# Optimization experiments

Hardware: AMD Instinct MI355X
Metric: run time of the kernel (lower is better)

The kernel has to match this reference:

```python
import jax, jax.numpy as jnp
import numpy as np

SPLINE_ORDER = 3
GRID_SIZE = 1
# efficient-kan style grid over [-1,1], extended by spline_order on each side; h = 2/grid_size = 2
GRID = jnp.arange(-SPLINE_ORDER, GRID_SIZE + SPLINE_ORDER + 1, dtype=jnp.float32) * 2.0 - 1.0
NB = GRID_SIZE + SPLINE_ORDER  # 4 basis functions per input feature
EPS = 1e-5


def b_splines(x, grid):
    # x: [..., in] -> [..., in, NB] via Cox-de Boor recursion
    xe = x[..., None]
    b = ((xe >= grid[:-1]) & (xe < grid[1:])).astype(x.dtype)
    for p in range(1, SPLINE_ORDER + 1):
        b = ((xe - grid[:-(p + 1)]) / (grid[p:-1] - grid[:-(p + 1)]) * b[..., :-1]
             + (grid[p + 1:] - xe) / (grid[p + 1:] - grid[1:-p]) * b[..., 1:])
    return b


def kan_linear(x, base_w, spline_w):
    # base branch: silu(x) @ W_base^T ; spline branch: B(x) contracted with W_spline [out,in,NB]
    base = jnp.einsum('...i,oi->...o', jax.nn.silu(x), base_w)
    sp = jnp.einsum('...ik,oik->...o', b_splines(x, GRID), spline_w)
    return base + sp


def kan_conv2x2(x, base_w, spline_w):
    # x: [B,C,H,W] -> [B,C_out,H-1,W-1]
    p = jax.lax.conv_general_dilated_patches(x, (2, 2), (1, 1), 'VALID')  # [B, C*4, H', W']
    p = jnp.moveaxis(p, 1, -1)  # [B,H',W',C*4]
    y = kan_linear(p, base_w, spline_w)  # [B,H',W',C_out]
    return jnp.moveaxis(y, -1, 1)


def bn2d(x, g, b):
    m = x.mean((0, 2, 3), keepdims=True)
    v = x.var((0, 2, 3), keepdims=True)
    return (x - m) * jax.lax.rsqrt(v + EPS) * g[None, :, None, None] + b[None, :, None, None]


def bn1d(x, g, b):
    m = x.mean(0, keepdims=True)
    v = x.var(0, keepdims=True)
    return (x - m) * jax.lax.rsqrt(v + EPS) * g[None, :] + b[None, :]


def maxpool2(x):
    B, C, H, W = x.shape
    Hc, Wc = (H // 2) * 2, (W // 2) * 2
    return x[:, :, :Hc, :Wc].reshape(B, C, H // 2, 2, W // 2, 2).max((3, 5))


def setup_inputs() -> dict:
    key = jax.random.key(0)
    ks = jax.random.split(key, 16)
    f32 = jnp.float32
    d = {
        'x': jax.random.normal(ks[0], (1024, 3, 32, 32), f32),
        'base_w1': jax.random.normal(ks[1], (32, 12), f32) * 0.2,
        'spline_w1': jax.random.normal(ks[2], (32, 12, NB), f32) * 0.1,
        'bn1_g': jnp.ones((32,), f32), 'bn1_b': jnp.zeros((32,), f32),
        'base_w2': jax.random.normal(ks[3], (64, 128), f32) * 0.08,
        'spline_w2': jax.random.normal(ks[4], (64, 128, NB), f32) * 0.04,
        'bn2_g': jnp.ones((64,), f32), 'bn2_b': jnp.zeros((64,), f32),
        'fc1_w': jax.random.normal(ks[5], (64, 3136), f32) * 0.02,
        'fc1_b': jnp.zeros((64,), f32),
        'bn3_g': jnp.ones((64,), f32), 'bn3_b': jnp.zeros((64,), f32),
        'fc2_w': jax.random.normal(ks[6], (10, 64), f32) * 0.1,
        'fc2_b': jnp.zeros((10,), f32),
    }
    return d


def reference(x, base_w1, spline_w1, bn1_g, bn1_b, base_w2, spline_w2, bn2_g, bn2_b,
              fc1_w, fc1_b, bn3_g, bn3_b, fc2_w, fc2_b):
    h = kan_conv2x2(x, base_w1, spline_w1)            # [B,32,31,31]
    h = jax.nn.relu(bn2d(h, bn1_g, bn1_b))
    h = maxpool2(h)                                   # [B,32,15,15]
    h = kan_conv2x2(h, base_w2, spline_w2)            # [B,64,14,14]
    h = jax.nn.relu(bn2d(h, bn2_g, bn2_b))
    h = maxpool2(h)                                   # [B,64,7,7]
    h = h.reshape(h.shape[0], -1)                     # [B,3136]
    h = h @ fc1_w.T + fc1_b
    h = jax.nn.relu(bn1d(h, bn3_g, bn3_b))
    # Dropout is identity at inference
    return h @ fc2_w.T + fc2_b                        # [B,10]
```

## Files before the change

kernel.cpp:

```cpp
#include <hip/hip_runtime.h>
#include <math.h>

#define BN_EPS 1e-5f

typedef __attribute__((ext_vector_type(8))) _Float16 f16x8;
typedef __attribute__((ext_vector_type(4))) _Float16 f16x4;
typedef __attribute__((ext_vector_type(2))) __fp16 fp16v2;
typedef __attribute__((ext_vector_type(4))) float f32x4;


__device__ __forceinline__ float siluf(float v) {
    return v * __builtin_amdgcn_rcpf(1.0f + __expf(-v));
}

__device__ __forceinline__ void expand5(float v, float f[5]) {
    f[0] = siluf(v);
    float u = (v + 7.0f) * 0.5f;
#pragma unroll
    for (int i = 0; i < 4; ++i) {
        float a = fabsf(u - (float)(i + 2));
        float p = fmaxf(2.0f - a, 0.0f);
        float q = fmaxf(1.0f - a, 0.0f);
        f[i + 1] = p * p * p - 4.0f * (q * q * q);
    }
}

__device__ __forceinline__ int pkh(float a, float b) {
    union { fp16v2 h2; int i; } u;
    u.h2 = __builtin_amdgcn_cvt_pkrtz(a, b);
    return u.i;
}


__global__ __launch_bounds__(256) void prep_kernel(
        const float* __restrict__ fw1, unsigned int* __restrict__ wTh2,
        const float* __restrict__ bw2, const float* __restrict__ sw2,
        _Float16* __restrict__ Wf,
        const float* __restrict__ bw1, const float* __restrict__ sw1,
        _Float16* __restrict__ Wf1) {
    int blk = blockIdx.x;
    if (blk < 392) {
        int t = blk * 256 + threadIdx.x;
        int o = t & 63;
        int j2 = t >> 6;
        int jc = (j2 * 2) & 63;
        int q2 = (j2 * 2) >> 6;
        wTh2[t] = (unsigned int)pkh(fw1[(size_t)o * 3136 + jc * 49 + q2],
                                    fw1[(size_t)o * 3136 + (jc + 1) * 49 + q2]);
    } else if (blk < 552) {
        int t = (blk - 392) * 256 + threadIdx.x;
        if (t >= 64 * 640) return;
        int n = t / 640;
        int k = t - n * 640;
        int s = k / 160;
        int r = k - s * 160;
        int f = r >> 5;
        int c = r & 31;
        float val = (f == 0) ? bw2[n * 128 + c * 4 + s]
                             : sw2[n * 512 + c * 16 + s * 4 + (f - 1)] * (1.0f / 6.0f);
        Wf[t] = (_Float16)val;
    } else {
        int t = (blk - 552) * 256 + threadIdx.x;
        if (t >= 32 * 64) return;
        int n = t >> 6;
        int k = t & 63;
        int s = k >> 4, j = k & 15;
        float val = 0.f;
        if (j < 15) {
            int f = j / 3, c = j - f * 3;
            int i = c * 4 + s;
            val = (f == 0) ? bw1[n * 12 + i]
                           : sw1[(n * 12 + i) * 4 + f - 1] * (1.0f / 6.0f);
        }
        Wf1[t] = (_Float16)val;
    }
}


__global__ __launch_bounds__(256, 4) void conv1_kernel(
        const float* __restrict__ x, const _Float16* __restrict__ Wf1,
        _Float16* __restrict__ pooled, float* __restrict__ part) {
    __shared__ _Float16 Eu[1025 * 16];
    __shared__ float Rs[4][64];
    char* EuB = (char*)Eu;

    int t = threadIdx.x;
    int lane = t & 63, wv = t >> 6;
    int quad = lane >> 4, l15 = lane & 15;
    int b = blockIdx.x;

    const _Float16* wb0 = Wf1 + (size_t)l15 * 64 + quad * 8;
    f16x8 bf00 = *(const f16x8*)(wb0);
    f16x8 bf01 = *(const f16x8*)(wb0 + 32);
    f16x8 bf10 = *(const f16x8*)(wb0 + 16 * 64);
    f16x8 bf11 = *(const f16x8*)(wb0 + 16 * 64 + 32);

    float xv[12];
    const float* xb = x + (size_t)b * 3072;
#pragma unroll
    for (int k = 0; k < 12; ++k) xv[k] = xb[t + k * 256];
#pragma unroll
    for (int k = 0; k < 12; ++k) {
        int idx = t + k * 256;
        int c = idx >> 10;
        int pos = idx & 1023;
        float f[5];
        expand5(xv[k], f);
        int rb = pos * 32;
        int key = (pos & 12) << 2;
        *(_Float16*)(EuB + ((rb + c * 2) ^ key))        = (_Float16)f[0];
        *(_Float16*)(EuB + ((rb + (3 + c) * 2) ^ key))  = (_Float16)f[1];
        *(_Float16*)(EuB + ((rb + (6 + c) * 2) ^ key))  = (_Float16)f[2];
        *(_Float16*)(EuB + ((rb + (9 + c) * 2) ^ key))  = (_Float16)f[3];
        *(_Float16*)(EuB + ((rb + (12 + c) * 2) ^ key)) = (_Float16)f[4];
    }
    if (t < 8) *(int*)(EuB + 32768 + t * 4) = 0;
    __syncthreads();

    int dxq = quad >> 1, hb = (quad & 1) * 16;
    int wxv = 8 * wv + (l15 & 7);
    int colb = wxv + dxq;
    int pbase = (colb * 32 + hb) ^ ((colb & 12) << 2);
    bool vx = wxv < 31;
    int pzero = 32768 + hb;
    int wy0 = l15 >> 3;

    float ss0 = 0.f, sq0 = 0.f, ss1 = 0.f, sq1 = 0.f;

    int p0 = vx ? wy0 * 1024 + pbase : pzero;
    f16x8 a0 = *(const f16x8*)(EuB + p0);
    f16x8 a1 = *(const f16x8*)(EuB + p0 + (vx ? 1024 : 0));

#pragma unroll 1
    for (int i = 0; i < 16; ++i) {
        f32x4 acc0 = (f32x4){0.f, 0.f, 0.f, 0.f};
        f32x4 acc1 = (f32x4){0.f, 0.f, 0.f, 0.f};
        acc0 = __builtin_amdgcn_mfma_f32_16x16x32_f16(a0, bf00, acc0, 0, 0, 0);
        acc1 = __builtin_amdgcn_mfma_f32_16x16x32_f16(a0, bf10, acc1, 0, 0, 0);
        acc0 = __builtin_amdgcn_mfma_f32_16x16x32_f16(a1, bf01, acc0, 0, 0, 0);
        acc1 = __builtin_amdgcn_mfma_f32_16x16x32_f16(a1, bf11, acc1, 0, 0, 0);
        if (i < 15) {
            int wyn = 2 * (i + 1) + wy0;
            bool vn = vx && (wyn < 31);
            int pn = vn ? wyn * 1024 + pbase : pzero;
            a0 = *(const f16x8*)(EuB + pn);
            a1 = *(const f16x8*)(EuB + pn + (vn ? 1024 : 0));
        }
        float h00 = fmaxf(acc0[0], acc0[1]);
        float h01 = fmaxf(acc0[2], acc0[3]);
        float h10 = fmaxf(acc1[0], acc1[1]);
        float h11 = fmaxf(acc1[2], acc1[3]);
        float g00 = fmaxf(h00, __shfl_down(h00, 32, 64));
        float g01 = fmaxf(h01, __shfl_down(h01, 32, 64));
        float g10 = fmaxf(h10, __shfl_down(h10, 32, 64));
        float g11 = fmaxf(h11, __shfl_down(h11, 32, 64));
        if (lane < 32 && i < 15) {
            int pn0 = 4 * wv + (quad & 1) * 2;
            size_t base = ((size_t)b * 225 + i * 15) * 32;
            if (pn0 < 15) {
                pooled[base + pn0 * 32 + l15]      = (_Float16)g00;
                pooled[base + pn0 * 32 + 16 + l15] = (_Float16)g10;
            }
            if (pn0 < 14) {
                pooled[base + (pn0 + 1) * 32 + l15]      = (_Float16)g01;
                pooled[base + (pn0 + 1) * 32 + 16 + l15] = (_Float16)g11;
            }
        }
        ss0 += acc0[0] + acc0[1] + acc0[2] + acc0[3];
        sq0 += acc0[0] * acc0[0] + acc0[1] * acc0[1]
             + acc0[2] * acc0[2] + acc0[3] * acc0[3];
        ss1 += acc1[0] + acc1[1] + acc1[2] + acc1[3];
        sq1 += acc1[0] * acc1[0] + acc1[1] * acc1[1]
             + acc1[2] * acc1[2] + acc1[3] * acc1[3];
    }

    ss0 += __shfl_down(ss0, 32, 64); ss0 += __shfl_down(ss0, 16, 64);
    sq0 += __shfl_down(sq0, 32, 64); sq0 += __shfl_down(sq0, 16, 64);
    ss1 += __shfl_down(ss1, 32, 64); ss1 += __shfl_down(ss1, 16, 64);
    sq1 += __shfl_down(sq1, 32, 64); sq1 += __shfl_down(sq1, 16, 64);
    if (lane < 16) {
        Rs[wv][2 * l15]          = ss0;
        Rs[wv][2 * l15 + 1]      = sq0;
        Rs[wv][32 + 2 * l15]     = ss1;
        Rs[wv][32 + 2 * l15 + 1] = sq1;
    }
    __syncthreads();
    if (t < 64)
        part[(size_t)b * 64 + t] = Rs[0][t] + Rs[1][t] + Rs[2][t] + Rs[3][t];
}


#define EU_PS 200

__device__ __forceinline__ void c2_loadb(const _Float16* __restrict__ Wb,
                                         int g, f16x8 bf[5]) {
#pragma unroll
    for (int ks = 0; ks < 5; ++ks)
        bf[ks] = *(const f16x8*)(Wb + g * 160 + ks * 32);
}

__device__ __forceinline__ void c2_mfma(const _Float16* Eu,
                                        const int abase[4][4], int g,
                                        int quad, const f16x8 bf[5],
                                        f32x4 acc[4]) {
#pragma unroll
    for (int ks = 0; ks < 5; ++ks) {
        int jo = ks * 40 + quad * 8;
#pragma unroll
        for (int mt = 0; mt < 4; ++mt) {
            f16x8 a = *(const f16x8*)&Eu[abase[mt][g] + jo];
            acc[mt] = __builtin_amdgcn_mfma_f32_16x16x32_f16(a, bf[ks], acc[mt], 0, 0, 0);
        }
    }
}

__global__ __launch_bounds__(256, 6) void conv2_kernel(
        const _Float16* __restrict__ pooled, const float* __restrict__ stats1,
        const float* __restrict__ g1v, const float* __restrict__ b1v,
        const _Float16* __restrict__ Wf, _Float16* __restrict__ Pt,
        float* __restrict__ part) {
    __shared__ _Float16 Eu[65 * EU_PS];

    int t = threadIdx.x;
    int lane = t & 63, wv = t >> 6;
    int quad = lane >> 4, l15 = lane & 15;

    int blk = blockIdx.x;
    int b = blk >> 2;
    int py0 = ((blk >> 1) & 1) * 7;
    int px0 = (blk & 1) * 7;

    const _Float16* Wb = Wf + (size_t)(wv * 16 + l15) * 640 + quad * 8;
    f16x8 bfA[5], bfB[5];
    c2_loadb(Wb, 0, bfA);

    {
        int c2 = t & 15, c0 = c2 * 2;
        int xx = (t >> 4) & 7;
        int yh = t >> 7;
        const float invN1 = 1.0f / (1024.0f * 961.0f);
        float m0 = stats1[2 * c0] * invN1;
        float v0 = stats1[2 * c0 + 1] * invN1 - m0 * m0;
        float sc0 = rsqrtf(v0 + BN_EPS) * g1v[c0];
        float sh0 = b1v[c0] - m0 * sc0;
        float m1 = stats1[2 * c0 + 2] * invN1;
        float v1 = stats1[2 * c0 + 3] * invN1 - m1 * m1;
        float sc1 = rsqrtf(v1 + BN_EPS) * g1v[c0 + 1];
        float sh1 = b1v[c0 + 1] - m1 * sc1;
        const _Float16* pbase0 =
            pooled + ((size_t)b * 225 + py0 * 15 + px0) * 32 + c0;
#pragma unroll
        for (int yi = 0; yi < 4; ++yi) {
            int yr = yh * 4 + yi;
            fp16v2 v2 = *(const fp16v2*)(pbase0 + yr * 480 + xx * 32);
            float va = fmaxf((float)v2.x * sc0 + sh0, 0.f);
            float vb = fmaxf((float)v2.y * sc1 + sh1, 0.f);
            float fa[5], fb5[5];
            expand5(va, fa);
            expand5(vb, fb5);
            int* eb = (int*)&Eu[(yr * 8 + xx) * EU_PS] + c2;
            eb[0]  = pkh(fa[0], fb5[0]);
            eb[20] = pkh(fa[1], fb5[1]);
            eb[40] = pkh(fa[2], fb5[2]);
            eb[60] = pkh(fa[3], fb5[3]);
            eb[80] = pkh(fa[4], fb5[4]);
        }
    }
    if (t < 100) ((int*)&Eu[64 * EU_PS])[t] = 0;

    int abase[4][4];
#pragma unroll
    for (int mt = 0; mt < 4; ++mt) {
        int m = mt * 16 + l15;
        if (m < 49) {
            int pr = m / 7, pc = m - pr * 7;
#pragma unroll
            for (int s = 0; s < 4; ++s)
                abase[mt][s] = ((pr + (s >> 1)) * 8 + pc + (s & 1)) * EU_PS;
        } else {
#pragma unroll
            for (int s = 0; s < 4; ++s) abase[mt][s] = 64 * EU_PS;
        }
    }
    __syncthreads();

    f32x4 acc[4];
#pragma unroll
    for (int mt = 0; mt < 4; ++mt) acc[mt] = (f32x4){0.f, 0.f, 0.f, 0.f};

    c2_loadb(Wb, 1, bfB);
    c2_mfma(Eu, abase, 0, quad, bfA, acc);
    c2_loadb(Wb, 2, bfA);
    c2_mfma(Eu, abase, 1, quad, bfB, acc);
    c2_loadb(Wb, 3, bfB);
    c2_mfma(Eu, abase, 2, quad, bfA, acc);
    c2_mfma(Eu, abase, 3, quad, bfB, acc);

    int o = wv * 16 + l15;
#pragma unroll
    for (int mt = 0; mt < 4; ++mt) {
#pragma unroll
        for (int reg = 0; reg < 4; ++reg) {
            int m = mt * 16 + quad * 4 + reg;
            if (m < 49) {
                int pr = m / 7, pc = m - pr * 7;
                int patch = (b * 14 + py0 + pr) * 14 + px0 + pc;
                Pt[(size_t)patch * 64 + o] = (_Float16)acc[mt][reg];
            }
        }
    }
    float s = 0.f, s2 = 0.f;
#pragma unroll
    for (int mt = 0; mt < 4; ++mt)
#pragma unroll
        for (int reg = 0; reg < 4; ++reg) {
            float a = acc[mt][reg];
            s += a;
            s2 += a * a;
        }
    s  += __shfl_down(s, 16, 64);  s  += __shfl_down(s, 32, 64);
    s2 += __shfl_down(s2, 16, 64); s2 += __shfl_down(s2, 32, 64);
    if (lane < 16) {
        part[(size_t)blk * 128 + 2 * o]     = s;
        part[(size_t)blk * 128 + 2 * o + 1] = s2;
    }
}


__global__ __launch_bounds__(256) void redstats_kernel(
        const float* __restrict__ part, float* __restrict__ stats,
        int nblk, int stride) {
    int p = blockIdx.x;
    float s = 0.f;
    for (int j = threadIdx.x; j < nblk; j += 256)
        s += part[(size_t)j * stride + p];
#pragma unroll
    for (int off = 32; off > 0; off >>= 1) s += __shfl_down(s, off, 64);
    __shared__ float ls[4];
    if ((threadIdx.x & 63) == 0) ls[threadIdx.x >> 6] = s;
    __syncthreads();
    if (threadIdx.x == 0) stats[p] = ls[0] + ls[1] + ls[2] + ls[3];
}


__global__ __launch_bounds__(256) void bnpool2_kernel(
        const _Float16* __restrict__ Pt, const float* __restrict__ stats,
        const float* __restrict__ g, const float* __restrict__ bb,
        _Float16* __restrict__ out) {
    int t = blockIdx.x * 256 + threadIdx.x;
    if (t >= 1024 * 49 * 16) return;
    int c4 = (t & 15) * 4;
    int q2 = (t >> 4) % 49;
    int b  = t / (49 * 16);
    float sc[4], sh[4];
#pragma unroll
    for (int j = 0; j < 4; ++j) {
        int c = c4 + j;
        float mean = stats[2 * c] * (1.0f / 200704.0f);
        float var  = stats[2 * c + 1] * (1.0f / 200704.0f) - mean * mean;
        sc[j] = rsqrtf(var + BN_EPS) * g[c];
        sh[j] = bb[c] - mean * sc[j];
    }
    int py2 = q2 / 7, px2 = q2 - py2 * 7;
    int q = (py2 * 2) * 14 + px2 * 2;
    const _Float16* p = Pt + ((size_t)b * 196 + q) * 64 + c4;
    f16x4 r0 = *(const f16x4*)(p);
    f16x4 r1 = *(const f16x4*)(p + 64);
    f16x4 r2 = *(const f16x4*)(p + 14 * 64);
    f16x4 r3 = *(const f16x4*)(p + 15 * 64);
    f16x4 res;
#pragma unroll
    for (int j = 0; j < 4; ++j) {
        float v0 = fmaxf((float)r0[j] * sc[j] + sh[j], 0.f);
        float v1 = fmaxf((float)r1[j] * sc[j] + sh[j], 0.f);
        float v2 = fmaxf((float)r2[j] * sc[j] + sh[j], 0.f);
        float v3 = fmaxf((float)r3[j] * sc[j] + sh[j], 0.f);
        res[j] = (_Float16)fmaxf(fmaxf(v0, v1), fmaxf(v2, v3));
    }
    *(f16x4*)(out + (size_t)b * 3136 + q2 * 64 + c4) = res;
}


__global__ __launch_bounds__(256) void fc1_kernel(
        const _Float16* __restrict__ xin, const unsigned int* __restrict__ wTh2,
        const float* __restrict__ bias, float* __restrict__ z) {
    __shared__ unsigned int xsu[2 * 1568];
    __shared__ float red[2][4][64];
    int b0 = blockIdx.x * 2;
    const unsigned int* xg = (const unsigned int*)xin + (size_t)b0 * 1568;
    for (int j = threadIdx.x; j < 2 * 1568; j += 256) xsu[j] = xg[j];
    __syncthreads();
    int o = threadIdx.x & 63, q = threadIdx.x >> 6;
    float s0 = 0.f, s1 = 0.f;
    const unsigned int* wp = wTh2 + (size_t)q * 392 * 64 + o;
    int jb = q * 392;
    for (int i = 0; i < 392; ++i) {
        union { unsigned int u; fp16v2 h; } uw, u0, u1;
        uw.u = wp[i * 64];
        u0.u = xsu[jb + i];
        u1.u = xsu[1568 + jb + i];
        s0 = __builtin_amdgcn_fdot2(u0.h, uw.h, s0, false);
        s1 = __builtin_amdgcn_fdot2(u1.h, uw.h, s1, false);
    }
    red[0][q][o] = s0; red[1][q][o] = s1;
    __syncthreads();
    if (threadIdx.x < 128) {
        int bb = threadIdx.x >> 6;
        int oo = threadIdx.x & 63;
        float tot = red[bb][0][oo] + red[bb][1][oo] + red[bb][2][oo]
                  + red[bb][3][oo] + bias[oo];
        z[((size_t)(b0 + bb)) * 64 + oo] = tot;
    }
}


__global__ __launch_bounds__(256) void colstats_kernel(
        const float* __restrict__ z, const float* __restrict__ g,
        const float* __restrict__ bb, float* __restrict__ scsh) {
    int c = blockIdx.x;
    float s = 0.f, s2 = 0.f;
    for (int b = threadIdx.x; b < 1024; b += 256) {
        float v = z[(size_t)b * 64 + c];
        s += v; s2 += v * v;
    }
#pragma unroll
    for (int off = 32; off > 0; off >>= 1) {
        s  += __shfl_down(s, off, 64);
        s2 += __shfl_down(s2, off, 64);
    }
    __shared__ float ls[8];
    int w = threadIdx.x >> 6;
    if ((threadIdx.x & 63) == 0) { ls[w * 2] = s; ls[w * 2 + 1] = s2; }
    __syncthreads();
    if (threadIdx.x == 0) {
        float st = ls[0] + ls[2] + ls[4] + ls[6];
        float st2 = ls[1] + ls[3] + ls[5] + ls[7];
        float mean = st * (1.0f / 1024.0f);
        float var  = st2 * (1.0f / 1024.0f) - mean * mean;
        float sc = rsqrtf(var + BN_EPS) * g[c];
        scsh[2 * c]     = sc;
        scsh[2 * c + 1] = bb[c] - mean * sc;
    }
}


__global__ __launch_bounds__(256) void final_kernel(
        const float* __restrict__ z, const float* __restrict__ scsh,
        const float* __restrict__ w2, const float* __restrict__ b2,
        float* __restrict__ out) {
    int t = blockIdx.x * 256 + threadIdx.x;
    if (t >= 10240) return;
    int o = t % 10, b = t / 10;
    float acc = b2[o];
#pragma unroll 8
    for (int c = 0; c < 64; ++c) {
        float a = fmaxf(z[(size_t)b * 64 + c] * scsh[2 * c] + scsh[2 * c + 1], 0.f);
        acc += a * w2[o * 64 + c];
    }
    out[t] = acc;
}


extern "C" void kernel_launch(void* const* d_in, const int* in_sizes, int n_in,
                              void* d_out, int out_size, void* d_ws, size_t ws_size,
                              hipStream_t stream) {
    const float* x   = (const float*)d_in[0];
    const float* bw1 = (const float*)d_in[1];
    const float* sw1 = (const float*)d_in[2];
    const float* g1  = (const float*)d_in[3];
    const float* b1  = (const float*)d_in[4];
    const float* bw2 = (const float*)d_in[5];
    const float* sw2 = (const float*)d_in[6];
    const float* g2  = (const float*)d_in[7];
    const float* b2v = (const float*)d_in[8];
    const float* fw1 = (const float*)d_in[9];
    const float* fb1 = (const float*)d_in[10];
    const float* g3  = (const float*)d_in[11];
    const float* b3  = (const float*)d_in[12];
    const float* fw2 = (const float*)d_in[13];
    const float* fb2 = (const float*)d_in[14];
    float* out = (float*)d_out;

    char* ws = (char*)d_ws;
    float* part1     = (float*)(ws);
    _Float16* Pt     = (_Float16*)(ws);
    float* part2     = (float*)(ws + 51380224);
    _Float16* Wf     = (_Float16*)(ws + 100000000);
    _Float16* Wf1    = (_Float16*)(ws + 100131072);
    _Float16* pooled = (_Float16*)(ws + 125960192);
    float* z         = (float*)(ws + 155451392);
    unsigned int* wTh2 = (unsigned int*)(ws + 155713536);
    float* stats1    = (float*)(ws + 156516352);
    float* stats2    = (float*)(ws + 156516608);
    float* stats3    = (float*)(ws + 156517120);

    prep_kernel<<<560, 256, 0, stream>>>(fw1, wTh2, bw2, sw2, Wf, bw1, sw1, Wf1);

    conv1_kernel<<<1024, 256, 0, stream>>>(x, Wf1, pooled, part1);
    redstats_kernel<<<64, 256, 0, stream>>>(part1, stats1, 1024, 64);

    conv2_kernel<<<4096, 256, 0, stream>>>(pooled, stats1, g1, b1,
                                           Wf, Pt, part2);
    redstats_kernel<<<128, 256, 0, stream>>>(part2, stats2, 4096, 128);

    _Float16* pooled2 = pooled;
    bnpool2_kernel<<<(1024 * 49 * 16 + 255) / 256, 256, 0, stream>>>(
        Pt, stats2, g2, b2v, pooled2);

    fc1_kernel<<<512, 256, 0, stream>>>(pooled2, wTh2, fb1, z);
    colstats_kernel<<<64, 256, 0, stream>>>(z, g3, b3, stats3);
    final_kernel<<<(10240 + 255) / 256, 256, 0, stream>>>(z, stats3, fw2, fb2, out);
}
```

Baseline: 190.2 us.

## Use 32x32 MFMA tiles in conv2 and parallelize stats reduction with atomics

Conv2 now uses 32x32x16 MFMA with a 2x2 wave split over rows and output channels, and a software-pipelined loop that prefetches the next A and B fragments. The aim is to cut LDS reads and redundant weight loads per MFMA and raise matrix-core efficiency. Partial stats are combined in shared memory before being written. The redstats kernel now does a coalesced, grid-wide strided sum followed by atomicAdd into stats that prep_kernel zeroes, replacing strided per-column loops that used few blocks. This makes float summation order nondeterministic.

```diff
diff --git a/kernel.cpp b/kernel.cpp
--- a/kernel.cpp
+++ b/kernel.cpp
@@ -7,6 +7,7 @@
 typedef __attribute__((ext_vector_type(4))) _Float16 f16x4;
 typedef __attribute__((ext_vector_type(2))) __fp16 fp16v2;
 typedef __attribute__((ext_vector_type(4))) float f32x4;
+typedef __attribute__((ext_vector_type(16))) float f32x16;
 
 
 __device__ __forceinline__ float siluf(float v) {
@@ -37,7 +38,8 @@
         const float* __restrict__ bw2, const float* __restrict__ sw2,
         _Float16* __restrict__ Wf,
         const float* __restrict__ bw1, const float* __restrict__ sw1,
-        _Float16* __restrict__ Wf1) {
+        _Float16* __restrict__ Wf1,
+        float* __restrict__ stats1, float* __restrict__ stats2) {
     int blk = blockIdx.x;
     if (blk < 392) {
         int t = blk * 256 + threadIdx.x;
@@ -60,7 +62,12 @@
                              : sw2[n * 512 + c * 16 + s * 4 + (f - 1)] * (1.0f / 6.0f);
         Wf[t] = (_Float16)val;
     } else {
-        int t = (blk - 552) * 256 + threadIdx.x;
+        int tid = threadIdx.x;
+        if (blk == 559) {
+            if (tid < 64) stats1[tid] = 0.f;
+            else if (tid < 192) stats2[tid - 64] = 0.f;
+        }
+        int t = (blk - 552) * 256 + tid;
         if (t >= 32 * 64) return;
         int n = t >> 6;
         int k = t & 63;
@@ -192,47 +199,26 @@
 
 #define EU_PS 200
 
-__device__ __forceinline__ void c2_loadb(const _Float16* __restrict__ Wb,
-                                         int g, f16x8 bf[5]) {
-#pragma unroll
-    for (int ks = 0; ks < 5; ++ks)
-        bf[ks] = *(const f16x8*)(Wb + g * 160 + ks * 32);
-}
-
-__device__ __forceinline__ void c2_mfma(const _Float16* Eu,
-                                        const int abase[4][4], int g,
-                                        int quad, const f16x8 bf[5],
-                                        f32x4 acc[4]) {
-#pragma unroll
-    for (int ks = 0; ks < 5; ++ks) {
-        int jo = ks * 40 + quad * 8;
-#pragma unroll
-        for (int mt = 0; mt < 4; ++mt) {
-            f16x8 a = *(const f16x8*)&Eu[abase[mt][g] + jo];
-            acc[mt] = __builtin_amdgcn_mfma_f32_16x16x32_f16(a, bf[ks], acc[mt], 0, 0, 0);
-        }
-    }
-}
-
 __global__ __launch_bounds__(256, 6) void conv2_kernel(
         const _Float16* __restrict__ pooled, const float* __restrict__ stats1,
         const float* __restrict__ g1v, const float* __restrict__ b1v,
         const _Float16* __restrict__ Wf, _Float16* __restrict__ Pt,
         float* __restrict__ part) {
     __shared__ _Float16 Eu[65 * EU_PS];
+    __shared__ float Rs[4][64];
 
     int t = threadIdx.x;
     int lane = t & 63, wv = t >> 6;
-    int quad = lane >> 4, l15 = lane & 15;
+    int l31 = lane & 31, kl = (lane >> 5) * 8;
+    int mw = wv >> 1, nw = wv & 1;
 
     int blk = blockIdx.x;
     int b = blk >> 2;
     int py0 = ((blk >> 1) & 1) * 7;
     int px0 = (blk & 1) * 7;
 
-    const _Float16* Wb = Wf + (size_t)(wv * 16 + l15) * 640 + quad * 8;
-    f16x8 bfA[5], bfB[5];
-    c2_loadb(Wb, 0, bfA);
+    const _Float16* Wb = Wf + (size_t)(nw * 32 + l31) * 640 + kl;
+    f16x8 bF = *(const f16x8*)(Wb);
 
     {
         int c2 = t & 15, c0 = c2 * 2;
@@ -268,78 +254,86 @@
     }
     if (t < 100) ((int*)&Eu[64 * EU_PS])[t] = 0;
 
-    int abase[4][4];
-#pragma unroll
-    for (int mt = 0; mt < 4; ++mt) {
-        int m = mt * 16 + l15;
+    int arow = mw * 32 + l31;
+    int abase[4];
+    if (arow < 49) {
+        int pr = arow / 7, pc = arow - pr * 7;
+#pragma unroll
+        for (int s = 0; s < 4; ++s)
+            abase[s] = ((pr + (s >> 1)) * 8 + pc + (s & 1)) * EU_PS + kl;
+    } else {
+#pragma unroll
+        for (int s = 0; s < 4; ++s) abase[s] = 64 * EU_PS + kl;
+    }
+    __syncthreads();
+
+    f32x16 acc;
+#pragma unroll
+    for (int i = 0; i < 16; ++i) acc[i] = 0.f;
+
+    f16x8 aF = *(const f16x8*)&Eu[abase[0]];
+    f16x8 aN, bN;
+#pragma unroll
+    for (int kk = 0; kk < 40; ++kk) {
+        if (kk < 39) {
+            const int k2 = kk + 1;
+            const int s2 = k2 / 10, r2 = k2 - s2 * 10, f2 = r2 >> 1, c2 = r2 & 1;
+            aN = *(const f16x8*)&Eu[abase[s2] + f2 * 40 + c2 * 16];
+            bN = *(const f16x8*)(Wb + s2 * 160 + f2 * 32 + c2 * 16);
+        }
+        acc = __builtin_amdgcn_mfma_f32_32x32x16_f16(aF, bF, acc, 0, 0, 0);
+        aF = aN;
+        bF = bN;
+    }
+
+    int col = nw * 32 + l31;
+#pragma unroll
+    for (int r = 0; r < 16; ++r) {
+        int rloc = (r & 3) + 8 * (r >> 2) + 4 * (lane >> 5);
+        int m = mw * 32 + rloc;
         if (m < 49) {
             int pr = m / 7, pc = m - pr * 7;
-#pragma unroll
-            for (int s = 0; s < 4; ++s)
-                abase[mt][s] = ((pr + (s >> 1)) * 8 + pc + (s & 1)) * EU_PS;
-        } else {
-#pragma unroll
-            for (int s = 0; s < 4; ++s) abase[mt][s] = 64 * EU_PS;
-        }
-    }
-    __syncthreads();
-
-    f32x4 acc[4];
-#pragma unroll
-    for (int mt = 0; mt < 4; ++mt) acc[mt] = (f32x4){0.f, 0.f, 0.f, 0.f};
-
-    c2_loadb(Wb, 1, bfB);
-    c2_mfma(Eu, abase, 0, quad, bfA, acc);
-    c2_loadb(Wb, 2, bfA);
-    c2_mfma(Eu, abase, 1, quad, bfB, acc);
-    c2_loadb(Wb, 3, bfB);
-    c2_mfma(Eu, abase, 2, quad, bfA, acc);
-    c2_mfma(Eu, abase, 3, quad, bfB, acc);
-
-    int o = wv * 16 + l15;
-#pragma unroll
-    for (int mt = 0; mt < 4; ++mt) {
-#pragma unroll
-        for (int reg = 0; reg < 4; ++reg) {
-            int m = mt * 16 + quad * 4 + reg;
-            if (m < 49) {
-                int pr = m / 7, pc = m - pr * 7;
-                int patch = (b * 14 + py0 + pr) * 14 + px0 + pc;
-                Pt[(size_t)patch * 64 + o] = (_Float16)acc[mt][reg];
-            }
+            int patch = (b * 14 + py0 + pr) * 14 + px0 + pc;
+            Pt[(size_t)patch * 64 + col] = (_Float16)acc[r];
         }
     }
     float s = 0.f, s2 = 0.f;
 #pragma unroll
-    for (int mt = 0; mt < 4; ++mt)
-#pragma unroll
-        for (int reg = 0; reg < 4; ++reg) {
-            float a = acc[mt][reg];
-            s += a;
-            s2 += a * a;
-        }
-    s  += __shfl_down(s, 16, 64);  s  += __shfl_down(s, 32, 64);
-    s2 += __shfl_down(s2, 16, 64); s2 += __shfl_down(s2, 32, 64);
-    if (lane < 16) {
-        part[(size_t)blk * 128 + 2 * o]     = s;
-        part[(size_t)blk * 128 + 2 * o + 1] = s2;
+    for (int r = 0; r < 16; ++r) {
+        float a = acc[r];
+        s += a;
+        s2 += a * a;
+    }
+    s  += __shfl_down(s, 32, 64);
+    s2 += __shfl_down(s2, 32, 64);
+    if (lane < 32) {
+        Rs[wv][2 * l31]     = s;
+        Rs[wv][2 * l31 + 1] = s2;
+    }
+    __syncthreads();
+    if (t < 128) {
+        int o = t >> 1;
+        int nwv = o >> 5;
+        int lidx = (o & 31) * 2 + (t & 1);
+        part[(size_t)blk * 128 + t] = Rs[nwv][lidx] + Rs[nwv + 2][lidx];
     }
 }
 
 
 __global__ __launch_bounds__(256) void redstats_kernel(
         const float* __restrict__ part, float* __restrict__ stats,
-        int nblk, int stride) {
-    int p = blockIdx.x;
-    float s = 0.f;
-    for (int j = threadIdx.x; j < nblk; j += 256)
-        s += part[(size_t)j * stride + p];
-#pragma unroll
-    for (int off = 32; off > 0; off >>= 1) s += __shfl_down(s, off, 64);
-    __shared__ float ls[4];
-    if ((threadIdx.x & 63) == 0) ls[threadIdx.x >> 6] = s;
-    __syncthreads();
-    if (threadIdx.x == 0) stats[p] = ls[0] + ls[1] + ls[2] + ls[3];
+        int total, int width) {
+    float acc = 0.f;
+    for (int i = blockIdx.x * 256 + threadIdx.x; i < total; i += gridDim.x * 256)
+        acc += part[i];
+    __shared__ float ls[256];
+    ls[threadIdx.x] = acc;
+    __syncthreads();
+    if (threadIdx.x < width) {
+        float v = ls[threadIdx.x];
+        for (int j = threadIdx.x + width; j < 256; j += width) v += ls[j];
+        atomicAdd(&stats[threadIdx.x], v);
+    }
 }
 
 
@@ -494,14 +488,15 @@
     float* stats2    = (float*)(ws + 156516608);
     float* stats3    = (float*)(ws + 156517120);
 
-    prep_kernel<<<560, 256, 0, stream>>>(fw1, wTh2, bw2, sw2, Wf, bw1, sw1, Wf1);
+    prep_kernel<<<560, 256, 0, stream>>>(fw1, wTh2, bw2, sw2, Wf, bw1, sw1, Wf1,
+                                         stats1, stats2);
 
     conv1_kernel<<<1024, 256, 0, stream>>>(x, Wf1, pooled, part1);
-    redstats_kernel<<<64, 256, 0, stream>>>(part1, stats1, 1024, 64);
+    redstats_kernel<<<256, 256, 0, stream>>>(part1, stats1, 1024 * 64, 64);
 
     conv2_kernel<<<4096, 256, 0, stream>>>(pooled, stats1, g1, b1,
                                            Wf, Pt, part2);
-    redstats_kernel<<<128, 256, 0, stream>>>(part2, stats2, 4096, 128);
+    redstats_kernel<<<512, 256, 0, stream>>>(part2, stats2, 4096 * 128, 128);
 
     _Float16* pooled2 = pooled;
     bnpool2_kernel<<<(1024 * 49 * 16 + 255) / 256, 256, 0, stream>>>(
```

Measured after the change: 239.7 us. 26.0% more time.
